# Kernel tuning notes

Measured on AMD Instinct MI355X. Metric: run time of the kernel, lower is better.

The kernel has to match this reference:

```python
import jax, jax.numpy as jnp
import numpy as np

D = 512
H = 8
HD = D // H
S = 2048
B = 4


def setup_inputs() -> dict:
    key = jax.random.key(0)
    ks = jax.random.split(key, 8)
    scale = 1.0 / np.sqrt(D)
    x = jax.random.normal(ks[0], (S, B, D), dtype=jnp.float32)
    head_mask = jax.random.normal(ks[1], (H, S, S), dtype=jnp.float32)
    value_gate = jax.random.uniform(ks[2], (1, B, 1), dtype=jnp.float32)
    # nn.MultiheadAttention parameters
    in_proj_w = jax.random.normal(ks[3], (3 * D, D), dtype=jnp.float32) * scale
    in_proj_b = jnp.zeros((3 * D,), dtype=jnp.float32)
    out_proj_w = jax.random.normal(ks[4], (D, D), dtype=jnp.float32) * scale
    out_proj_b = jnp.zeros((D,), dtype=jnp.float32)
    return {
        "x": x,
        "head_mask": head_mask,
        "value_gate": value_gate,
        "in_proj_w": in_proj_w,
        "in_proj_b": in_proj_b,
        "out_proj_w": out_proj_w,
        "out_proj_b": out_proj_b,
    }


def reference(x, head_mask, value_gate, in_proj_w, in_proj_b, out_proj_w, out_proj_b):
    # x: (S, B, D); head_mask: (H, S, S) additive; value_gate: (1, B, 1)
    v_in = x * value_gate  # value gating before projection
    wq, wk, wv = in_proj_w[:D], in_proj_w[D:2 * D], in_proj_w[2 * D:]
    bq, bk, bv = in_proj_b[:D], in_proj_b[D:2 * D], in_proj_b[2 * D:]
    q = x @ wq.T + bq            # (S, B, D)
    k = x @ wk.T + bk
    v = v_in @ wv.T + bv
    # split D into H heads of size HD (matches torch's view(S, B*H, HD))
    q = q.reshape(S, B, H, HD)
    k = k.reshape(S, B, H, HD)
    v = v.reshape(S, B, H, HD)
    scores = jnp.einsum('sbhd,tbhd->bhst', q, k) / np.sqrt(HD).astype(np.float32)
    scores = scores + head_mask[None]  # broadcast per-head mask over batch
    attn = jax.nn.softmax(scores, axis=-1)  # (B, H, S, S)
    out = jnp.einsum('bhst,tbhd->sbhd', attn, v).reshape(S, B, D)
    return out @ out_proj_w.T + out_proj_b
```

## Files before the change

kernel.cpp:

```cpp
#include <hip/hip_runtime.h>
#include <cstdint>
#include <cstddef>

typedef _Float16 half8 __attribute__((ext_vector_type(8)));
typedef _Float16 half4 __attribute__((ext_vector_type(4)));
typedef float f32x4 __attribute__((ext_vector_type(4)));

#define MFMA16(A,B,C) __builtin_amdgcn_mfma_f32_16x16x32_f16(A,B,C,0,0,0)

__device__ __forceinline__ void gll16(const void* g, void* l) {
    __builtin_amdgcn_global_load_lds(
        (const __attribute__((address_space(1))) void*)g,
        (__attribute__((address_space(3))) void*)l, 16, 0, 0);
}

__global__ __launch_bounds__(256) void cvt_f16(
    const float* __restrict__ X, const float* __restrict__ Wi, const float* __restrict__ Wo,
    _Float16* __restrict__ Xh, _Float16* __restrict__ Wih, _Float16* __restrict__ Woh)
{
    const size_t i8 = ((size_t)blockIdx.x * 256 + threadIdx.x) * 8;
    const size_t NX = (size_t)4194304, NWI = 786432;
    const float* src; _Float16* dst; size_t off;
    if (i8 < NX) { src = X; dst = Xh; off = i8; }
    else if (i8 < NX + NWI) { src = Wi; dst = Wih; off = i8 - NX; }
    else { src = Wo; dst = Woh; off = i8 - NX - NWI; }
    f32x4 v0 = *(const f32x4*)(src + off);
    f32x4 v1 = *(const f32x4*)(src + off + 4);
    half8 r;
    r[0]=(_Float16)v0[0]; r[1]=(_Float16)v0[1]; r[2]=(_Float16)v0[2]; r[3]=(_Float16)v0[3];
    r[4]=(_Float16)v1[0]; r[5]=(_Float16)v1[1]; r[6]=(_Float16)v1[2]; r[7]=(_Float16)v1[3];
    *(half8*)(dst + off) = r;
}

__global__ __launch_bounds__(256) void qkv_mfma(
    const _Float16* __restrict__ X, const _Float16* __restrict__ W,
    const float* __restrict__ bias, const float* __restrict__ gate,
    _Float16* __restrict__ Qo, _Float16* __restrict__ Ko, _Float16* __restrict__ Vt)
{
    __shared__ _Float16 As[128][72];
    __shared__ _Float16 Bs[64][72];
    const int tid = threadIdx.x;
    const int lane = tid & 63, wv = tid >> 6;
    const int l15 = lane & 15, g = lane >> 4;
    const int wr = wv >> 1, wc = wv & 1;
    const int j0 = blockIdx.x * 64, r0 = blockIdx.y * 128;
    f32x4 acc[4][2] = {};
    const int arow = tid >> 1, ahf = tid & 1;
    const int brow = tid >> 2, bc = tid & 3;
    for (int k0 = 0; k0 < 512; k0 += 64) {
        const _Float16* srca = X + (size_t)(r0 + arow) * 512 + k0 + ahf * 32;
#pragma unroll
        for (int c = 0; c < 4; ++c)
            *(half8*)&As[arow][ahf * 32 + c * 8] = *(const half8*)(srca + c * 8);
        const _Float16* srcb = W + (size_t)(j0 + brow) * 512 + k0 + bc * 16;
#pragma unroll
        for (int c = 0; c < 2; ++c)
            *(half8*)&Bs[brow][bc * 16 + c * 8] = *(const half8*)(srcb + c * 8);
        __syncthreads();
#pragma unroll
        for (int kt = 0; kt < 2; ++kt) {
            half8 bf0 = *(half8*)&Bs[32 * wc + l15][kt * 32 + g * 8];
            half8 bf1 = *(half8*)&Bs[32 * wc + 16 + l15][kt * 32 + g * 8];
#pragma unroll
            for (int ri = 0; ri < 4; ++ri) {
                half8 af = *(half8*)&As[64 * wr + 16 * ri + l15][kt * 32 + g * 8];
                acc[ri][0] = MFMA16(af, bf0, acc[ri][0]);
                acc[ri][1] = MFMA16(af, bf1, acc[ri][1]);
            }
        }
        __syncthreads();
    }
#pragma unroll
    for (int ri = 0; ri < 4; ++ri) {
#pragma unroll
        for (int cj = 0; cj < 2; ++cj) {
            const int col = j0 + 32 * wc + 16 * cj + l15;
            const int sec = col >> 9, hh = (col >> 6) & 7, d = col & 63;
            const float bv = bias[col];
#pragma unroll
            for (int r = 0; r < 4; ++r) {
                const int row = r0 + 64 * wr + 16 * ri + 4 * g + r;
                const int b = row & 3, s = row >> 2;
                const float v = acc[ri][cj][r];
                if (sec == 0)
                    Qo[((size_t)(b * 8 + hh) * 2048 + s) * 64 + d] = (_Float16)((v + bv) * 0.125f);
                else if (sec == 1)
                    Ko[((size_t)(b * 8 + hh) * 2048 + s) * 64 + d] = (_Float16)(v + bv);
                else {
                    const int ps = (s & ~31) | ((s & 12) << 1) | ((s & 16) >> 2) | (s & 3);
                    Vt[((size_t)(b * 8 + hh) * 64 + d) * 2048 + ps] = (_Float16)(v * gate[b] + bv);
                }
            }
        }
    }
}

__global__ __launch_bounds__(512) void attn_mfma(
    const _Float16* __restrict__ Q, const _Float16* __restrict__ K,
    const _Float16* __restrict__ V, const float* __restrict__ M,
    _Float16* __restrict__ P0, _Float16* __restrict__ P1, float* __restrict__ Lb)
{
    __shared__ _Float16 Kl[2][4][32][64];
    __shared__ _Float16 Vl[2][4][64][32];
    __shared__ float    Mlds[2][128][64];
    const int tid = threadIdx.x;
    const int lane = tid & 63, w = tid >> 6;
    const int l15 = lane & 15, g = lane >> 4;
    const int bid = blockIdx.x;
    const int kvh = bid & 1, h = (bid >> 1) & 7, qg = bid >> 4;
    const int b = w & 3, qh = w >> 2;
    const int q0 = qg * 128 + qh * 64;
    const size_t bh = (size_t)b * 8 + h;
    const _Float16* Qp = Q + bh * 2048 * 64;
    const _Float16* Kp = K + (bh * 2048 + (size_t)kvh * 1024) * 64;
    const _Float16* Vp = V + bh * 64 * 2048 + kvh * 1024;
    const float* Mp = M + (size_t)h * 2048 * 2048 + kvh * 1024;

    half8 qf[4][2];
#pragma unroll
    for (int qj = 0; qj < 4; ++qj)
#pragma unroll
        for (int dh = 0; dh < 2; ++dh)
            qf[qj][dh] = *(const half8*)(Qp + (size_t)(q0 + 16 * qj + l15) * 64 + dh * 32 + g * 8);

    const bool stK = (w < 4);
    const int bs = w & 3;
    const int krow = lane >> 3, kblk = lane & 7;
    const int vrow = lane >> 2, vblk = lane & 3;
    const int ksw = (kblk ^ (krow & 7)) * 8;
    const int vsw = (vblk ^ ((vrow >> 1) & 3)) * 8;

    const int mrow_in = lane >> 4;
    const int mch = lane & 15;

    if (stK) {
#pragma unroll
        for (int c = 0; c < 4; ++c)
            gll16(Kp + (size_t)(c * 8 + krow) * 64 + ksw, &Kl[0][bs][c * 8][0]);
    } else {
#pragma unroll
        for (int c = 0; c < 4; ++c)
            gll16(Vp + (size_t)(c * 16 + vrow) * 2048 + vsw, &Vl[0][bs][c * 16][0]);
    }
#pragma unroll
    for (int c = 0; c < 4; ++c) {
        const int row = w * 16 + c * 4 + mrow_in;
        const int srcch = mch ^ (row & 7);
        gll16(Mp + (size_t)(qg * 128 + row) * 2048 + srcch * 4, &Mlds[0][w * 16 + c * 4][0]);
    }

    f32x4 O[4][4] = {};
    float l[4] = {0.f, 0.f, 0.f, 0.f};
    __syncthreads();

    const int msw = l15 & 7;

    for (int tl = 0; tl < 32; ++tl) {
        const int cur = tl & 1;
        const int sup = tl >> 1, sub = tl & 1;
        const int mcur = sup & 1;
        if (tl < 31) {
            const int tg = (tl + 1) * 32;
            if (stK) {
#pragma unroll
                for (int c = 0; c < 4; ++c)
                    gll16(Kp + (size_t)(tg + c * 8 + krow) * 64 + ksw,
                          &Kl[cur ^ 1][bs][c * 8][0]);
            } else {
#pragma unroll
                for (int c = 0; c < 4; ++c)
                    gll16(Vp + (size_t)(c * 16 + vrow) * 2048 + tg + vsw,
                          &Vl[cur ^ 1][bs][c * 16][0]);
            }
        }
        if (sub == 0 && tl < 30) {
            const int toff = (sup + 1) * 64;
#pragma unroll
            for (int c = 0; c < 4; ++c) {
                const int row = w * 16 + c * 4 + mrow_in;
                const int srcch = mch ^ (row & 7);
                gll16(Mp + (size_t)(qg * 128 + row) * 2048 + toff + srcch * 4,
                      &Mlds[mcur ^ 1][w * 16 + c * 4][0]);
            }
        }

        f32x4 St[2][4];
#pragma unroll
        for (int mi = 0; mi < 2; ++mi) {
            const int row = 16 * mi + l15;
            half8 kf0 = *(half8*)&Kl[cur][b][row][((g) ^ (l15 & 7)) * 8];
            half8 kf1 = *(half8*)&Kl[cur][b][row][((4 + g) ^ (l15 & 7)) * 8];
#pragma unroll
            for (int qj = 0; qj < 4; ++qj) {
                const f32x4 ci = *(const f32x4*)
                    &Mlds[mcur][qh * 64 + 16 * qj + l15][((sub * 8 + mi * 4 + g) ^ msw) * 4];
                St[mi][qj] = MFMA16(kf0, qf[qj][0], ci);
                St[mi][qj] = MFMA16(kf1, qf[qj][1], St[mi][qj]);
            }
        }

        half8 pf[4];
#pragma unroll
        for (int qj = 0; qj < 4; ++qj) {
            float e0 = __expf(St[0][qj][0]), e1 = __expf(St[0][qj][1]);
            float e2 = __expf(St[0][qj][2]), e3 = __expf(St[0][qj][3]);
            float e4 = __expf(St[1][qj][0]), e5 = __expf(St[1][qj][1]);
            float e6 = __expf(St[1][qj][2]), e7 = __expf(St[1][qj][3]);
            l[qj] += ((e0 + e1) + (e2 + e3)) + ((e4 + e5) + (e6 + e7));
            half8 pp;
            pp[0] = (_Float16)e0; pp[1] = (_Float16)e1; pp[2] = (_Float16)e2; pp[3] = (_Float16)e3;
            pp[4] = (_Float16)e4; pp[5] = (_Float16)e5; pp[6] = (_Float16)e6; pp[7] = (_Float16)e7;
            pf[qj] = pp;
        }

#pragma unroll
        for (int di = 0; di < 4; ++di) {
            const int row = 16 * di + l15;
            half8 vf = *(half8*)&Vl[cur][b][row][(g ^ ((l15 >> 1) & 3)) * 8];
#pragma unroll
            for (int qj = 0; qj < 4; ++qj)
                O[di][qj] = MFMA16(vf, pf[qj], O[di][qj]);
        }

        __syncthreads();
    }

    _Float16* P = kvh ? P1 : P0;
#pragma unroll
    for (int qj = 0; qj < 4; ++qj) {
        float lt = l[qj];
        lt += __shfl_xor(lt, 16);
        lt += __shfl_xor(lt, 32);
        const float inv = 1.0f / lt;
        const int q = q0 + 16 * qj + l15;
        const int r = q * 4 + b;
        _Float16* dst = P + (size_t)r * 512 + h * 64;
#pragma unroll
        for (int di = 0; di < 4; ++di) {
            half4 o;
            o[0] = (_Float16)(O[di][qj][0] * inv); o[1] = (_Float16)(O[di][qj][1] * inv);
            o[2] = (_Float16)(O[di][qj][2] * inv); o[3] = (_Float16)(O[di][qj][3] * inv);
            *(half4*)(dst + 16 * di + 4 * g) = o;
        }
        if (g == 0)
            Lb[(size_t)kvh * 65536 + r * 8 + h] = lt;
    }
}

__global__ __launch_bounds__(256) void merge_attn(
    const _Float16* __restrict__ P0, const _Float16* __restrict__ P1,
    const float* __restrict__ Lb, _Float16* __restrict__ AO)
{
    const size_t e = ((size_t)blockIdx.x * 256 + threadIdx.x) * 8;
    const int r = (int)(e >> 9);
    const int h = (int)((e & 511) >> 6);
    const int li = r * 8 + h;
    const float l0 = Lb[li], l1 = Lb[65536 + li];
    const float inv = 1.0f / (l0 + l1);
    const float a0 = l0 * inv, a1 = l1 * inv;
    half8 x0 = *(const half8*)(P0 + e);
    half8 x1 = *(const half8*)(P1 + e);
    half8 o;
#pragma unroll
    for (int i = 0; i < 8; ++i)
        o[i] = (_Float16)(a0 * (float)x0[i] + a1 * (float)x1[i]);
    *(half8*)(AO + e) = o;
}

__global__ __launch_bounds__(256) void oproj_mfma(
    const _Float16* __restrict__ A, const _Float16* __restrict__ W,
    const float* __restrict__ bias, float* __restrict__ Out)
{
    __shared__ _Float16 As[128][72];
    __shared__ _Float16 Bs[64][72];
    const int tid = threadIdx.x;
    const int lane = tid & 63, wv = tid >> 6;
    const int l15 = lane & 15, g = lane >> 4;
    const int wr = wv >> 1, wc = wv & 1;
    const int j0 = blockIdx.x * 64, r0 = blockIdx.y * 128;
    f32x4 acc[4][2] = {};
    const int arow = tid >> 1, ahf = tid & 1;
    const int brow = tid >> 2, bc = tid & 3;
    for (int k0 = 0; k0 < 512; k0 += 64) {
        const _Float16* srca = A + (size_t)(r0 + arow) * 512 + k0 + ahf * 32;
#pragma unroll
        for (int c = 0; c < 4; ++c)
            *(half8*)&As[arow][ahf * 32 + c * 8] = *(const half8*)(srca + c * 8);
        const _Float16* srcb = W + (size_t)(j0 + brow) * 512 + k0 + bc * 16;
#pragma unroll
        for (int c = 0; c < 2; ++c)
            *(half8*)&Bs[brow][bc * 16 + c * 8] = *(const half8*)(srcb + c * 8);
        __syncthreads();
#pragma unroll
        for (int kt = 0; kt < 2; ++kt) {
            half8 bf0 = *(half8*)&Bs[32 * wc + l15][kt * 32 + g * 8];
            half8 bf1 = *(half8*)&Bs[32 * wc + 16 + l15][kt * 32 + g * 8];
#pragma unroll
            for (int ri = 0; ri < 4; ++ri) {
                half8 af = *(half8*)&As[64 * wr + 16 * ri + l15][kt * 32 + g * 8];
                acc[ri][0] = MFMA16(af, bf0, acc[ri][0]);
                acc[ri][1] = MFMA16(af, bf1, acc[ri][1]);
            }
        }
        __syncthreads();
    }
#pragma unroll
    for (int ri = 0; ri < 4; ++ri) {
#pragma unroll
        for (int cj = 0; cj < 2; ++cj) {
            const int col = j0 + 32 * wc + 16 * cj + l15;
            const float bv = bias[col];
#pragma unroll
            for (int r = 0; r < 4; ++r) {
                const int row = r0 + 64 * wr + 16 * ri + 4 * g + r;
                Out[(size_t)row * 512 + col] = acc[ri][cj][r] + bv;
            }
        }
    }
}

extern "C" void kernel_launch(void* const* d_in, const int* in_sizes, int n_in,
                              void* d_out, int out_size, void* d_ws, size_t ws_size,
                              hipStream_t stream)
{
    (void)in_sizes; (void)n_in; (void)out_size; (void)ws_size;
    const float* X    = (const float*)d_in[0];
    const float* Mask = (const float*)d_in[1];
    const float* gate = (const float*)d_in[2];
    const float* Wi   = (const float*)d_in[3];
    const float* bi   = (const float*)d_in[4];
    const float* Wo   = (const float*)d_in[5];
    const float* bo   = (const float*)d_in[6];
    _Float16* ws = (_Float16*)d_ws;
    const size_t plane = (size_t)4 * 8 * 2048 * 64;
    _Float16* Qh  = ws;
    _Float16* Kh  = ws + plane;
    _Float16* Vt  = ws + 2 * plane;
    _Float16* AO  = ws + 3 * plane;
    _Float16* Xh  = ws + 4 * plane;
    _Float16* Wih = ws + 5 * plane;
    _Float16* Woh = ws + 5 * plane + 786432;
    _Float16* P0  = Xh;
    _Float16* P1  = ws + 5 * plane + 1048576;
    float*    Lb  = (float*)(P1 + plane);

    cvt_f16<<<dim3(2560), 256, 0, stream>>>(X, Wi, Wo, Xh, Wih, Woh);
    qkv_mfma<<<dim3(24, 64), 256, 0, stream>>>(Xh, Wih, bi, gate, Qh, Kh, Vt);
    attn_mfma<<<dim3(256), 512, 0, stream>>>(Qh, Kh, Vt, Mask, P0, P1, Lb);
    merge_attn<<<dim3(2048), 256, 0, stream>>>(P0, P1, Lb, AO);
    oproj_mfma<<<dim3(8, 64), 256, 0, stream>>>(AO, Woh, bo, (float*)d_out);
}
```

Measured before the change: 118.8 us.

## Drop LDS staging in attention; load K, V and mask directly from global

The attention kernel no longer stages K, V and the additive mask through double-buffered LDS with async global-to-LDS loads and per-tile barriers. Each wave now reads its MFMA operands straight from global memory. The grid changes to 512 blocks of 256 threads, one wave per batch element, and block indices are remapped so that heads and KV halves are spread across XCDs for better L2 locality. This removes LDS traffic and barriers and raises occupancy, but it loses the prefetch overlap and the sharing of the mask tile across the four batch waves, so each batch wave now reads the mask itself through the caches.

```diff
diff --git a/kernel.cpp b/kernel.cpp
--- a/kernel.cpp
+++ b/kernel.cpp
@@ -7,12 +7,6 @@
 typedef float f32x4 __attribute__((ext_vector_type(4)));
 
 #define MFMA16(A,B,C) __builtin_amdgcn_mfma_f32_16x16x32_f16(A,B,C,0,0,0)
-
-__device__ __forceinline__ void gll16(const void* g, void* l) {
-    __builtin_amdgcn_global_load_lds(
-        (const __attribute__((address_space(1))) void*)g,
-        (__attribute__((address_space(3))) void*)l, 16, 0, 0);
-}
 
 __global__ __launch_bounds__(256) void cvt_f16(
     const float* __restrict__ X, const float* __restrict__ Wi, const float* __restrict__ Wo,
@@ -95,21 +89,21 @@
     }
 }
 
-__global__ __launch_bounds__(512) void attn_mfma(
+__global__ __launch_bounds__(256) void attn_mfma(
     const _Float16* __restrict__ Q, const _Float16* __restrict__ K,
     const _Float16* __restrict__ V, const float* __restrict__ M,
     _Float16* __restrict__ P0, _Float16* __restrict__ P1, float* __restrict__ Lb)
 {
-    __shared__ _Float16 Kl[2][4][32][64];
-    __shared__ _Float16 Vl[2][4][64][32];
-    __shared__ float    Mlds[2][128][64];
     const int tid = threadIdx.x;
     const int lane = tid & 63, w = tid >> 6;
     const int l15 = lane & 15, g = lane >> 4;
     const int bid = blockIdx.x;
-    const int kvh = bid & 1, h = (bid >> 1) & 7, qg = bid >> 4;
-    const int b = w & 3, qh = w >> 2;
-    const int q0 = qg * 128 + qh * 64;
+    const int xcd = bid & 7, s = bid >> 3;
+    const int qg = s & 31, hi = s >> 5;
+    const int idx = xcd + 8 * hi;
+    const int h = idx >> 1, kvh = idx & 1;
+    const int q0 = qg * 64;
+    const int b = w;
     const size_t bh = (size_t)b * 8 + h;
     const _Float16* Qp = Q + bh * 2048 * 64;
     const _Float16* Kp = K + (bh * 2048 + (size_t)kvh * 1024) * 64;
@@ -123,106 +117,41 @@
         for (int dh = 0; dh < 2; ++dh)
             qf[qj][dh] = *(const half8*)(Qp + (size_t)(q0 + 16 * qj + l15) * 64 + dh * 32 + g * 8);
 
-    const bool stK = (w < 4);
-    const int bs = w & 3;
-    const int krow = lane >> 3, kblk = lane & 7;
-    const int vrow = lane >> 2, vblk = lane & 3;
-    const int ksw = (kblk ^ (krow & 7)) * 8;
-    const int vsw = (vblk ^ ((vrow >> 1) & 3)) * 8;
-
-    const int mrow_in = lane >> 4;
-    const int mch = lane & 15;
-
-    if (stK) {
-#pragma unroll
-        for (int c = 0; c < 4; ++c)
-            gll16(Kp + (size_t)(c * 8 + krow) * 64 + ksw, &Kl[0][bs][c * 8][0]);
-    } else {
-#pragma unroll
-        for (int c = 0; c < 4; ++c)
-            gll16(Vp + (size_t)(c * 16 + vrow) * 2048 + vsw, &Vl[0][bs][c * 16][0]);
-    }
-#pragma unroll
-    for (int c = 0; c < 4; ++c) {
-        const int row = w * 16 + c * 4 + mrow_in;
-        const int srcch = mch ^ (row & 7);
-        gll16(Mp + (size_t)(qg * 128 + row) * 2048 + srcch * 4, &Mlds[0][w * 16 + c * 4][0]);
-    }
-
     f32x4 O[4][4] = {};
     float l[4] = {0.f, 0.f, 0.f, 0.f};
-    __syncthreads();
-
-    const int msw = l15 & 7;
 
     for (int tl = 0; tl < 32; ++tl) {
-        const int cur = tl & 1;
-        const int sup = tl >> 1, sub = tl & 1;
-        const int mcur = sup & 1;
-        if (tl < 31) {
-            const int tg = (tl + 1) * 32;
-            if (stK) {
-#pragma unroll
-                for (int c = 0; c < 4; ++c)
-                    gll16(Kp + (size_t)(tg + c * 8 + krow) * 64 + ksw,
-                          &Kl[cur ^ 1][bs][c * 8][0]);
-            } else {
-#pragma unroll
-                for (int c = 0; c < 4; ++c)
-                    gll16(Vp + (size_t)(c * 16 + vrow) * 2048 + tg + vsw,
-                          &Vl[cur ^ 1][bs][c * 16][0]);
-            }
-        }
-        if (sub == 0 && tl < 30) {
-            const int toff = (sup + 1) * 64;
-#pragma unroll
-            for (int c = 0; c < 4; ++c) {
-                const int row = w * 16 + c * 4 + mrow_in;
-                const int srcch = mch ^ (row & 7);
-                gll16(Mp + (size_t)(qg * 128 + row) * 2048 + toff + srcch * 4,
-                      &Mlds[mcur ^ 1][w * 16 + c * 4][0]);
-            }
-        }
-
-        f32x4 St[2][4];
+        const int t0 = tl * 32;
+        half8 pf[4];
 #pragma unroll
         for (int mi = 0; mi < 2; ++mi) {
-            const int row = 16 * mi + l15;
-            half8 kf0 = *(half8*)&Kl[cur][b][row][((g) ^ (l15 & 7)) * 8];
-            half8 kf1 = *(half8*)&Kl[cur][b][row][((4 + g) ^ (l15 & 7)) * 8];
+            const _Float16* kr = Kp + (size_t)(t0 + 16 * mi + l15) * 64 + g * 8;
+            half8 kf0 = *(const half8*)(kr);
+            half8 kf1 = *(const half8*)(kr + 32);
+            f32x4 St[4];
 #pragma unroll
             for (int qj = 0; qj < 4; ++qj) {
                 const f32x4 ci = *(const f32x4*)
-                    &Mlds[mcur][qh * 64 + 16 * qj + l15][((sub * 8 + mi * 4 + g) ^ msw) * 4];
-                St[mi][qj] = MFMA16(kf0, qf[qj][0], ci);
-                St[mi][qj] = MFMA16(kf1, qf[qj][1], St[mi][qj]);
-            }
-        }
-
-        half8 pf[4];
-#pragma unroll
-        for (int qj = 0; qj < 4; ++qj) {
-            float e0 = __expf(St[0][qj][0]), e1 = __expf(St[0][qj][1]);
-            float e2 = __expf(St[0][qj][2]), e3 = __expf(St[0][qj][3]);
-            float e4 = __expf(St[1][qj][0]), e5 = __expf(St[1][qj][1]);
-            float e6 = __expf(St[1][qj][2]), e7 = __expf(St[1][qj][3]);
-            l[qj] += ((e0 + e1) + (e2 + e3)) + ((e4 + e5) + (e6 + e7));
-            half8 pp;
-            pp[0] = (_Float16)e0; pp[1] = (_Float16)e1; pp[2] = (_Float16)e2; pp[3] = (_Float16)e3;
-            pp[4] = (_Float16)e4; pp[5] = (_Float16)e5; pp[6] = (_Float16)e6; pp[7] = (_Float16)e7;
-            pf[qj] = pp;
-        }
-
+                    (Mp + (size_t)(q0 + 16 * qj + l15) * 2048 + t0 + 16 * mi + 4 * g);
+                St[qj] = MFMA16(kf0, qf[qj][0], ci);
+                St[qj] = MFMA16(kf1, qf[qj][1], St[qj]);
+            }
+#pragma unroll
+            for (int qj = 0; qj < 4; ++qj) {
+                float e0 = __expf(St[qj][0]), e1 = __expf(St[qj][1]);
+                float e2 = __expf(St[qj][2]), e3 = __expf(St[qj][3]);
+                l[qj] += (e0 + e1) + (e2 + e3);
+                pf[qj][4 * mi + 0] = (_Float16)e0; pf[qj][4 * mi + 1] = (_Float16)e1;
+                pf[qj][4 * mi + 2] = (_Float16)e2; pf[qj][4 * mi + 3] = (_Float16)e3;
+            }
+        }
 #pragma unroll
         for (int di = 0; di < 4; ++di) {
-            const int row = 16 * di + l15;
-            half8 vf = *(half8*)&Vl[cur][b][row][(g ^ ((l15 >> 1) & 3)) * 8];
+            half8 vf = *(const half8*)(Vp + (size_t)(16 * di + l15) * 2048 + t0 + g * 8);
 #pragma unroll
             for (int qj = 0; qj < 4; ++qj)
                 O[di][qj] = MFMA16(vf, pf[qj], O[di][qj]);
         }
-
-        __syncthreads();
     }
 
     _Float16* P = kvh ? P1 : P0;
@@ -346,7 +275,7 @@
 
     cvt_f16<<<dim3(2560), 256, 0, stream>>>(X, Wi, Wo, Xh, Wih, Woh);
     qkv_mfma<<<dim3(24, 64), 256, 0, stream>>>(Xh, Wih, bi, gate, Qh, Kh, Vt);
-    attn_mfma<<<dim3(256), 512, 0, stream>>>(Qh, Kh, Vt, Mask, P0, P1, Lb);
+    attn_mfma<<<dim3(512), 256, 0, stream>>>(Qh, Kh, Vt, Mask, P0, P1, Lb);
     merge_attn<<<dim3(2048), 256, 0, stream>>>(P0, P1, Lb, AO);
     oproj_mfma<<<dim3(8, 64), 256, 0, stream>>>(AO, Woh, bo, (float*)d_out);
 }
```

Result: slower. 187.6 us (+58.0%).
